# Kernel optimization log

Measured on AMD Instinct MI355X. Metric: run time of the kernel, lower is better.

## Reference

```python
import jax, jax.numpy as jnp
import numpy as np

VOXEL_RES = 4
CLASSES = 40


def setup_inputs() -> dict:
    key = jax.random.key(0)
    kx, kw, kb = jax.random.split(key, 3)
    B, N = 64, 100000
    x = jax.random.normal(kx, (B, N, 3), dtype=jnp.float32)
    F = VOXEL_RES ** 3
    bound = 1.0 / np.sqrt(F)  # torch Linear default init range
    W = jax.random.uniform(kw, (CLASSES, F), minval=-bound, maxval=bound, dtype=jnp.float32)
    b = jax.random.uniform(kb, (CLASSES,), minval=-bound, maxval=bound, dtype=jnp.float32)
    return {"x": x, "W": W, "b": b}


def reference(x, W, b):
    # x: (B, N, 3). Faithful to torch.histogramdd(bins=R): the histogram range
    # per dimension is [min, max] of the data; the last bin is right-inclusive.
    B, N, _ = x.shape
    R = VOXEL_RES
    mn = jnp.min(x, axis=1, keepdims=True)  # (B, 1, 3)
    mx = jnp.max(x, axis=1, keepdims=True)  # (B, 1, 3)
    # bin index = floor((v - min) / (max - min) * R), clipped so v == max -> R-1
    idx = jnp.floor((x - mn) / (mx - mn) * R).astype(jnp.int32)
    idx = jnp.clip(idx, 0, R - 1)  # (B, N, 3)
    flat = idx[..., 0] * R * R + idx[..., 1] * R + idx[..., 2]  # (B, N)
    flat = flat + (jnp.arange(B, dtype=jnp.int32) * (R ** 3))[:, None]
    counts = jax.ops.segment_sum(
        jnp.ones((B * N,), dtype=x.dtype), flat.reshape(-1), num_segments=B * R ** 3
    ).reshape(B, R ** 3)
    counts = counts / N  # fraction of points per voxel
    class_outputs = counts @ W.T + b  # (B, classes)
    return class_outputs
```

## Files before the change

kernel.cpp:

```cpp
#include <hip/hip_runtime.h>

#define VR 4
#define NVOX 64
#define NCLS 40
#define NB 64
#define NPTS 100000
#define BPB 16
#define G_PER_B (NPTS / 4)
#define F4_PER_B (NPTS * 3 / 4)

__device__ __forceinline__ unsigned fenc(float f) {
    unsigned u = __float_as_uint(f);
    return (u & 0x80000000u) ? ~u : (u ^ 0x80000000u);
}
__device__ __forceinline__ float fdec(unsigned e) {
    unsigned u = (e & 0x80000000u) ? (e ^ 0x80000000u) : ~e;
    return __uint_as_float(u);
}

__global__ __launch_bounds__(256) void minmax_k(const float4* __restrict__ x,
                                                unsigned* __restrict__ mn_enc,
                                                unsigned* __restrict__ mx_enc) {
    const int b = blockIdx.x / BPB;
    const int sub = blockIdx.x % BPB;
    const float4* xb = x + (size_t)b * F4_PER_B;

    float mn0 = 3.4e38f, mn1 = 3.4e38f, mn2 = 3.4e38f;
    float mx0 = -3.4e38f, mx1 = -3.4e38f, mx2 = -3.4e38f;

    for (int g = sub * 256 + (int)threadIdx.x; g < G_PER_B; g += BPB * 256) {
        float4 a = xb[3 * g];
        float4 c = xb[3 * g + 1];
        float4 e = xb[3 * g + 2];
        mn0 = fminf(mn0, fminf(fminf(a.x, a.w), fminf(c.z, e.y)));
        mx0 = fmaxf(mx0, fmaxf(fmaxf(a.x, a.w), fmaxf(c.z, e.y)));
        mn1 = fminf(mn1, fminf(fminf(a.y, c.x), fminf(c.w, e.z)));
        mx1 = fmaxf(mx1, fmaxf(fmaxf(a.y, c.x), fmaxf(c.w, e.z)));
        mn2 = fminf(mn2, fminf(fminf(a.z, c.y), fminf(e.x, e.w)));
        mx2 = fmaxf(mx2, fmaxf(fmaxf(a.z, c.y), fmaxf(e.x, e.w)));
    }

    #pragma unroll
    for (int off = 32; off > 0; off >>= 1) {
        mn0 = fminf(mn0, __shfl_down(mn0, off, 64));
        mn1 = fminf(mn1, __shfl_down(mn1, off, 64));
        mn2 = fminf(mn2, __shfl_down(mn2, off, 64));
        mx0 = fmaxf(mx0, __shfl_down(mx0, off, 64));
        mx1 = fmaxf(mx1, __shfl_down(mx1, off, 64));
        mx2 = fmaxf(mx2, __shfl_down(mx2, off, 64));
    }

    __shared__ float smn[4][3], smx[4][3];
    const int lane = threadIdx.x & 63;
    const int wv = threadIdx.x >> 6;
    if (lane == 0) {
        smn[wv][0] = mn0; smn[wv][1] = mn1; smn[wv][2] = mn2;
        smx[wv][0] = mx0; smx[wv][1] = mx1; smx[wv][2] = mx2;
    }
    __syncthreads();
    if (threadIdx.x < 3) {
        const int d = threadIdx.x;
        float a = smn[0][d], z = smx[0][d];
        #pragma unroll
        for (int w = 1; w < 4; w++) {
            a = fminf(a, smn[w][d]);
            z = fmaxf(z, smx[w][d]);
        }
        atomicMin(&mn_enc[b * 3 + d], fenc(a));
        atomicMax(&mx_enc[b * 3 + d], fenc(z));
    }
}

__device__ __forceinline__ int bin1(float v, float mn, float s4) {
    int i = (int)((v - mn) * s4);
    return i > (VR - 1) ? (VR - 1) : i;
}

__global__ __launch_bounds__(256) void hist_k(const float4* __restrict__ x,
                                              const unsigned* __restrict__ mn_enc,
                                              const unsigned* __restrict__ mx_enc,
                                              unsigned* __restrict__ hist) {
    const int b = blockIdx.x / BPB;
    const int sub = blockIdx.x % BPB;
    const float4* xb = x + (size_t)b * F4_PER_B;

    __shared__ unsigned lh[NVOX];
    if (threadIdx.x < NVOX) lh[threadIdx.x] = 0;

    float mnv[3], s4[3];
    #pragma unroll
    for (int d = 0; d < 3; d++) {
        float mnf = fdec(mn_enc[b * 3 + d]);
        float mxf = fdec(mx_enc[b * 3 + d]);
        mnv[d] = mnf;
        s4[d] = (float)VR / (mxf - mnf);
    }
    __syncthreads();

    for (int g = sub * 256 + (int)threadIdx.x; g < G_PER_B; g += BPB * 256) {
        float4 a = xb[3 * g];
        float4 c = xb[3 * g + 1];
        float4 e = xb[3 * g + 2];
        int v0 = bin1(a.x, mnv[0], s4[0]) * 16 + bin1(a.y, mnv[1], s4[1]) * 4 + bin1(a.z, mnv[2], s4[2]);
        int v1 = bin1(a.w, mnv[0], s4[0]) * 16 + bin1(c.x, mnv[1], s4[1]) * 4 + bin1(c.y, mnv[2], s4[2]);
        int v2 = bin1(c.z, mnv[0], s4[0]) * 16 + bin1(c.w, mnv[1], s4[1]) * 4 + bin1(e.x, mnv[2], s4[2]);
        int v3 = bin1(e.y, mnv[0], s4[0]) * 16 + bin1(e.z, mnv[1], s4[1]) * 4 + bin1(e.w, mnv[2], s4[2]);
        atomicAdd(&lh[v0], 1u);
        atomicAdd(&lh[v1], 1u);
        atomicAdd(&lh[v2], 1u);
        atomicAdd(&lh[v3], 1u);
    }
    __syncthreads();
    if (threadIdx.x < NVOX) atomicAdd(&hist[b * NVOX + threadIdx.x], lh[threadIdx.x]);
}

__global__ __launch_bounds__(256) void gemv_k(const unsigned* __restrict__ hist,
                                              const float* __restrict__ W,
                                              const float* __restrict__ bias,
                                              float* __restrict__ out) {
    int gid = blockIdx.x * 256 + threadIdx.x;
    if (gid >= NB * NCLS) return;
    int b = gid / NCLS;
    int c = gid - b * NCLS;
    const unsigned* h = hist + b * NVOX;
    const float* w = W + c * NVOX;
    float s = 0.f;
    #pragma unroll
    for (int f = 0; f < NVOX; f++) s += (float)h[f] * w[f];
    out[gid] = s * (1.0f / (float)NPTS) + bias[c];
}

extern "C" void kernel_launch(void* const* d_in, const int* in_sizes, int n_in,
                              void* d_out, int out_size, void* d_ws, size_t ws_size,
                              hipStream_t stream) {
    const float* x = (const float*)d_in[0];
    const float* W = (const float*)d_in[1];
    const float* bias = (const float*)d_in[2];
    float* out = (float*)d_out;

    unsigned* mn_enc = (unsigned*)d_ws;
    unsigned* mx_enc = mn_enc + NB * 3;
    unsigned* hist = mx_enc + NB * 3;

    hipMemsetAsync(d_ws, 0xFF, NB * 3 * sizeof(unsigned), stream);
    hipMemsetAsync((char*)d_ws + NB * 3 * sizeof(unsigned), 0,
                   (NB * 3 + NB * NVOX) * sizeof(unsigned), stream);

    minmax_k<<<NB * BPB, 256, 0, stream>>>((const float4*)x, mn_enc, mx_enc);
    hist_k<<<NB * BPB, 256, 0, stream>>>((const float4*)x, mn_enc, mx_enc, hist);
    gemv_k<<<(NB * NCLS + 255) / 256, 256, 0, stream>>>(hist, W, bias, out);
}
```

Baseline: 126.6 us.

## Replace atomics with per-block partials and ballot-based wave histogram, drop memsets

Minmax and histogram blocks now write per-block partial results instead of global atomics, so the two memset calls go away and each reduction is deterministic. The shared-memory atomic histogram is replaced by a wave-level ballot/popcount tally in which each lane owns one voxel bin, and the four waves' counts are summed afterwards. The gemv kernel now reduces the 16 partial histograms per batch and stages W in shared memory, running one block per batch. The tally costs six ballots plus mask arithmetic per point, which may be more instruction work than the LDS atomics it replaces.

```diff
diff --git a/kernel.cpp b/kernel.cpp
--- a/kernel.cpp
+++ b/kernel.cpp
@@ -8,36 +8,34 @@
 #define BPB 16
 #define G_PER_B (NPTS / 4)
 #define F4_PER_B (NPTS * 3 / 4)
-
-__device__ __forceinline__ unsigned fenc(float f) {
-    unsigned u = __float_as_uint(f);
-    return (u & 0x80000000u) ? ~u : (u ^ 0x80000000u);
-}
-__device__ __forceinline__ float fdec(unsigned e) {
-    unsigned u = (e & 0x80000000u) ? (e ^ 0x80000000u) : ~e;
-    return __uint_as_float(u);
-}
+#define STRIDE_G (BPB * 256)
+#define FLT_BIG 3.402823466e38f
 
 __global__ __launch_bounds__(256) void minmax_k(const float4* __restrict__ x,
-                                                unsigned* __restrict__ mn_enc,
-                                                unsigned* __restrict__ mx_enc) {
+                                                float* __restrict__ pmin,
+                                                float* __restrict__ pmax) {
     const int b = blockIdx.x / BPB;
     const int sub = blockIdx.x % BPB;
     const float4* xb = x + (size_t)b * F4_PER_B;
 
-    float mn0 = 3.4e38f, mn1 = 3.4e38f, mn2 = 3.4e38f;
-    float mx0 = -3.4e38f, mx1 = -3.4e38f, mx2 = -3.4e38f;
+    float mn0 = FLT_BIG, mn1 = FLT_BIG, mn2 = FLT_BIG;
+    float mx0 = -FLT_BIG, mx1 = -FLT_BIG, mx2 = -FLT_BIG;
 
-    for (int g = sub * 256 + (int)threadIdx.x; g < G_PER_B; g += BPB * 256) {
-        float4 a = xb[3 * g];
-        float4 c = xb[3 * g + 1];
-        float4 e = xb[3 * g + 2];
-        mn0 = fminf(mn0, fminf(fminf(a.x, a.w), fminf(c.z, e.y)));
-        mx0 = fmaxf(mx0, fmaxf(fmaxf(a.x, a.w), fmaxf(c.z, e.y)));
-        mn1 = fminf(mn1, fminf(fminf(a.y, c.x), fminf(c.w, e.z)));
-        mx1 = fmaxf(mx1, fmaxf(fmaxf(a.y, c.x), fmaxf(c.w, e.z)));
-        mn2 = fminf(mn2, fminf(fminf(a.z, c.y), fminf(e.x, e.w)));
-        mx2 = fmaxf(mx2, fmaxf(fmaxf(a.z, c.y), fmaxf(e.x, e.w)));
+    for (int base = sub * 256; base < G_PER_B; base += STRIDE_G) {
+        int g = base + (int)threadIdx.x;
+        bool valid = g < G_PER_B;
+        int gc = valid ? g : (G_PER_B - 1);
+        float4 a = xb[3 * gc];
+        float4 c = xb[3 * gc + 1];
+        float4 e = xb[3 * gc + 2];
+        if (valid) {
+            mn0 = fminf(mn0, fminf(fminf(a.x, a.w), fminf(c.z, e.y)));
+            mx0 = fmaxf(mx0, fmaxf(fmaxf(a.x, a.w), fmaxf(c.z, e.y)));
+            mn1 = fminf(mn1, fminf(fminf(a.y, c.x), fminf(c.w, e.z)));
+            mx1 = fmaxf(mx1, fmaxf(fmaxf(a.y, c.x), fmaxf(c.w, e.z)));
+            mn2 = fminf(mn2, fminf(fminf(a.z, c.y), fminf(e.x, e.w)));
+            mx2 = fmaxf(mx2, fmaxf(fmaxf(a.z, c.y), fmaxf(e.x, e.w)));
+        }
     }
 
     #pragma unroll
@@ -66,8 +64,8 @@
             a = fminf(a, smn[w][d]);
             z = fmaxf(z, smx[w][d]);
         }
-        atomicMin(&mn_enc[b * 3 + d], fenc(a));
-        atomicMax(&mx_enc[b * 3 + d], fenc(z));
+        pmin[(b * BPB + sub) * 3 + d] = a;
+        pmax[(b * BPB + sub) * 3 + d] = z;
     }
 }
 
@@ -76,58 +74,108 @@
     return i > (VR - 1) ? (VR - 1) : i;
 }
 
+__device__ __forceinline__ void tally(int v, unsigned long long vm,
+                                      const unsigned long long* ns,
+                                      unsigned& cnt) {
+    unsigned long long b0 = __ballot(v & 1);
+    unsigned long long b1 = __ballot(v & 2);
+    unsigned long long b2 = __ballot(v & 4);
+    unsigned long long b3 = __ballot(v & 8);
+    unsigned long long b4 = __ballot(v & 16);
+    unsigned long long b5 = __ballot(v & 32);
+    unsigned long long m = vm & (b0 ^ ns[0]) & (b1 ^ ns[1]) & (b2 ^ ns[2])
+                              & (b3 ^ ns[3]) & (b4 ^ ns[4]) & (b5 ^ ns[5]);
+    cnt += (unsigned)__popcll(m);
+}
+
 __global__ __launch_bounds__(256) void hist_k(const float4* __restrict__ x,
-                                              const unsigned* __restrict__ mn_enc,
-                                              const unsigned* __restrict__ mx_enc,
-                                              unsigned* __restrict__ hist) {
+                                              const float* __restrict__ pmin,
+                                              const float* __restrict__ pmax,
+                                              unsigned* __restrict__ phist) {
     const int b = blockIdx.x / BPB;
     const int sub = blockIdx.x % BPB;
     const float4* xb = x + (size_t)b * F4_PER_B;
+    const int lane = threadIdx.x & 63;
+    const int wv = threadIdx.x >> 6;
 
-    __shared__ unsigned lh[NVOX];
-    if (threadIdx.x < NVOX) lh[threadIdx.x] = 0;
-
-    float mnv[3], s4[3];
-    #pragma unroll
-    for (int d = 0; d < 3; d++) {
-        float mnf = fdec(mn_enc[b * 3 + d]);
-        float mxf = fdec(mx_enc[b * 3 + d]);
-        mnv[d] = mnf;
-        s4[d] = (float)VR / (mxf - mnf);
+    __shared__ float smm[6];
+    if (threadIdx.x < 6) {
+        int d = threadIdx.x % 3;
+        bool isMax = threadIdx.x >= 3;
+        float r = isMax ? -FLT_BIG : FLT_BIG;
+        for (int s = 0; s < BPB; s++) {
+            float v = isMax ? pmax[(b * BPB + s) * 3 + d]
+                            : pmin[(b * BPB + s) * 3 + d];
+            r = isMax ? fmaxf(r, v) : fminf(r, v);
+        }
+        smm[threadIdx.x] = r;
     }
     __syncthreads();
+    const float mn_0 = smm[0], mn_1 = smm[1], mn_2 = smm[2];
+    const float s4_0 = (float)VR / (smm[3] - smm[0]);
+    const float s4_1 = (float)VR / (smm[4] - smm[1]);
+    const float s4_2 = (float)VR / (smm[5] - smm[2]);
 
-    for (int g = sub * 256 + (int)threadIdx.x; g < G_PER_B; g += BPB * 256) {
-        float4 a = xb[3 * g];
-        float4 c = xb[3 * g + 1];
-        float4 e = xb[3 * g + 2];
-        int v0 = bin1(a.x, mnv[0], s4[0]) * 16 + bin1(a.y, mnv[1], s4[1]) * 4 + bin1(a.z, mnv[2], s4[2]);
-        int v1 = bin1(a.w, mnv[0], s4[0]) * 16 + bin1(c.x, mnv[1], s4[1]) * 4 + bin1(c.y, mnv[2], s4[2]);
-        int v2 = bin1(c.z, mnv[0], s4[0]) * 16 + bin1(c.w, mnv[1], s4[1]) * 4 + bin1(e.x, mnv[2], s4[2]);
-        int v3 = bin1(e.y, mnv[0], s4[0]) * 16 + bin1(e.z, mnv[1], s4[1]) * 4 + bin1(e.w, mnv[2], s4[2]);
-        atomicAdd(&lh[v0], 1u);
-        atomicAdd(&lh[v1], 1u);
-        atomicAdd(&lh[v2], 1u);
-        atomicAdd(&lh[v3], 1u);
+    unsigned long long ns[6];
+    #pragma unroll
+    for (int k = 0; k < 6; k++)
+        ns[k] = ((lane >> k) & 1) ? 0ull : ~0ull;
+
+    unsigned cnt = 0;
+    for (int base = sub * 256; base < G_PER_B; base += STRIDE_G) {
+        int g = base + (int)threadIdx.x;
+        bool valid = g < G_PER_B;
+        int gc = valid ? g : (G_PER_B - 1);
+        float4 a = xb[3 * gc];
+        float4 c = xb[3 * gc + 1];
+        float4 e = xb[3 * gc + 2];
+        unsigned long long vm = __ballot(valid);
+        int v0 = bin1(a.x, mn_0, s4_0) * 16 + bin1(a.y, mn_1, s4_1) * 4 + bin1(a.z, mn_2, s4_2);
+        int v1 = bin1(a.w, mn_0, s4_0) * 16 + bin1(c.x, mn_1, s4_1) * 4 + bin1(c.y, mn_2, s4_2);
+        int v2 = bin1(c.z, mn_0, s4_0) * 16 + bin1(c.w, mn_1, s4_1) * 4 + bin1(e.x, mn_2, s4_2);
+        int v3 = bin1(e.y, mn_0, s4_0) * 16 + bin1(e.z, mn_1, s4_1) * 4 + bin1(e.w, mn_2, s4_2);
+        tally(v0, vm, ns, cnt);
+        tally(v1, vm, ns, cnt);
+        tally(v2, vm, ns, cnt);
+        tally(v3, vm, ns, cnt);
     }
+
+    __shared__ unsigned swh[4][NVOX];
+    swh[wv][lane] = cnt;
     __syncthreads();
-    if (threadIdx.x < NVOX) atomicAdd(&hist[b * NVOX + threadIdx.x], lh[threadIdx.x]);
+    if (threadIdx.x < NVOX) {
+        phist[(b * BPB + sub) * NVOX + threadIdx.x] =
+            swh[0][threadIdx.x] + swh[1][threadIdx.x] +
+            swh[2][threadIdx.x] + swh[3][threadIdx.x];
+    }
 }
 
-__global__ __launch_bounds__(256) void gemv_k(const unsigned* __restrict__ hist,
+__global__ __launch_bounds__(256) void gemv_k(const unsigned* __restrict__ phist,
                                               const float* __restrict__ W,
                                               const float* __restrict__ bias,
                                               float* __restrict__ out) {
-    int gid = blockIdx.x * 256 + threadIdx.x;
-    if (gid >= NB * NCLS) return;
-    int b = gid / NCLS;
-    int c = gid - b * NCLS;
-    const unsigned* h = hist + b * NVOX;
-    const float* w = W + c * NVOX;
-    float s = 0.f;
-    #pragma unroll
-    for (int f = 0; f < NVOX; f++) s += (float)h[f] * w[f];
-    out[gid] = s * (1.0f / (float)NPTS) + bias[c];
+    const int b = blockIdx.x;
+    __shared__ float fh[NVOX];
+    __shared__ float sW[NCLS * NVOX];
+
+    if (threadIdx.x < NVOX) {
+        unsigned s = 0;
+        for (int p = 0; p < BPB; p++)
+            s += phist[(b * BPB + p) * NVOX + threadIdx.x];
+        fh[threadIdx.x] = (float)s * (1.0f / (float)NPTS);
+    }
+    for (int i = threadIdx.x; i < NCLS * NVOX; i += 256)
+        sW[i] = W[i];
+    __syncthreads();
+
+    if (threadIdx.x < NCLS) {
+        const int c = threadIdx.x;
+        float acc = 0.f;
+        #pragma unroll
+        for (int f = 0; f < NVOX; f++)
+            acc += fh[f] * sW[c * NVOX + f];
+        out[b * NCLS + c] = acc + bias[c];
+    }
 }
 
 extern "C" void kernel_launch(void* const* d_in, const int* in_sizes, int n_in,
@@ -138,15 +186,11 @@
     const float* bias = (const float*)d_in[2];
     float* out = (float*)d_out;
 
-    unsigned* mn_enc = (unsigned*)d_ws;
-    unsigned* mx_enc = mn_enc + NB * 3;
-    unsigned* hist = mx_enc + NB * 3;
+    float* pmin = (float*)d_ws;
+    float* pmax = pmin + NB * BPB * 3;
+    unsigned* phist = (unsigned*)(pmax + NB * BPB * 3);
 
-    hipMemsetAsync(d_ws, 0xFF, NB * 3 * sizeof(unsigned), stream);
-    hipMemsetAsync((char*)d_ws + NB * 3 * sizeof(unsigned), 0,
-                   (NB * 3 + NB * NVOX) * sizeof(unsigned), stream);
-
-    minmax_k<<<NB * BPB, 256, 0, stream>>>((const float4*)x, mn_enc, mx_enc);
-    hist_k<<<NB * BPB, 256, 0, stream>>>((const float4*)x, mn_enc, mx_enc, hist);
-    gemv_k<<<(NB * NCLS + 255) / 256, 256, 0, stream>>>(hist, W, bias, out);
+    minmax_k<<<NB * BPB, 256, 0, stream>>>((const float4*)x, pmin, pmax);
+    hist_k<<<NB * BPB, 256, 0, stream>>>((const float4*)x, pmin, pmax, phist);
+    gemv_k<<<NB, 256, 0, stream>>>(phist, W, bias, out);
 }
```

Measured after the change: 125.8 us. No clear change (-0.6%).
